# Performance work log

Hardware: AMD Instinct MI355X
Metric: run time of the kernel (lower is better)

Reference implementation:

```python
import jax, jax.numpy as jnp
import numpy as np

B, N, S = 8, 8192, 2048
IN, SKIP, OUT, EXP = 256, 128, 256, 4
GROUPS = 8


def conv1d(x, w, b):
    # 1x1 conv: x [B,C,N], w [O,C], b [O]
    return jnp.einsum('bcn,oc->bon', x, w) + b[None, :, None]


def group_norm(x, w, b, groups=GROUPS, eps=1e-5):
    Bb, C, Nn = x.shape
    xg = x.reshape(Bb, groups, C // groups, Nn)
    m = xg.mean(axis=(2, 3), keepdims=True)
    v = xg.var(axis=(2, 3), keepdims=True)
    xn = ((xg - m) * jax.lax.rsqrt(v + eps)).reshape(Bb, C, Nn)
    return xn * w[None, :, None] + b[None, :, None]


def _forward(xyz1, points1, xyz2, points2, t_emb, c_emb,
             mlp_w, mlp_b, mlp_gw, mlp_gb,
             c1w, c1b, g1w, g1b, c2w, c2b, g2w, g2b,
             tw, tb, cw, cb):
    # pairwise squared distances [B,N,S]
    dists = (-2.0 * jnp.einsum('bcn,bcm->bnm', xyz1, xyz2)
             + jnp.sum(xyz1 ** 2, axis=1)[:, :, None]
             + jnp.sum(xyz2 ** 2, axis=1)[:, None, :])
    neg_d3, idx = jax.lax.top_k(-dists, 3)          # 3 smallest distances
    d3 = -neg_d3                                     # [B,N,3]
    recip = 1.0 / (d3 + 1e-8)
    weight = recip / jnp.sum(recip, axis=2, keepdims=True)
    # gather neighbor features: points2 [B,C,S], idx [B,N,3] -> [B,C,N,3]
    gathered = jax.vmap(lambda p, i: p[:, i])(points2, idx)
    interp = jnp.sum(gathered * weight[:, None, :, :], axis=3)  # [B,IN,N]

    new_points = jnp.concatenate([points1, interp], axis=1)     # [B,IN+SKIP,N]
    x = jax.nn.silu(group_norm(conv1d(new_points, mlp_w, mlp_b), mlp_gw, mlp_gb))

    identity = x
    h = jax.nn.silu(group_norm(conv1d(x, c1w, c1b), g1w, g1b))
    h = group_norm(conv1d(h, c2w, c2b), g2w, g2b)
    st = t_emb @ tw.T + tb
    sc = c_emb @ cw.T + cb
    scale_t, shift_t = jnp.split(st, 2, axis=1)
    scale_c, shift_c = jnp.split(sc, 2, axis=1)
    scale = (scale_t + scale_c)[:, :, None]
    shift = (shift_t + shift_c)[:, :, None]
    h = h * (1.0 + scale) + shift
    return h + identity


def setup_inputs() -> dict:
    key = jax.random.key(0)
    ks = jax.random.split(key, 12)
    def rn(k, shape, s=1.0):
        return jax.random.normal(k, shape, dtype=jnp.float32) * s
    E = OUT * EXP
    return dict(
        xyz1=rn(ks[0], (B, 3, N)),
        points1=rn(ks[1], (B, SKIP, N)),
        xyz2=rn(ks[2], (B, 3, S)),
        points2=rn(ks[3], (B, IN, S)),
        t_emb=rn(ks[4], (B, OUT)),
        c_emb=rn(ks[5], (B, OUT)),
        mlp_w=rn(ks[6], (OUT, IN + SKIP), 0.02), mlp_b=jnp.zeros((OUT,), jnp.float32),
        mlp_gw=jnp.ones((OUT,), jnp.float32), mlp_gb=jnp.zeros((OUT,), jnp.float32),
        c1w=rn(ks[7], (E, OUT), 0.02), c1b=jnp.zeros((E,), jnp.float32),
        g1w=jnp.ones((E,), jnp.float32), g1b=jnp.zeros((E,), jnp.float32),
        c2w=rn(ks[8], (OUT, E), 0.02), c2b=jnp.zeros((OUT,), jnp.float32),
        g2w=jnp.ones((OUT,), jnp.float32), g2b=jnp.zeros((OUT,), jnp.float32),
        tw=rn(ks[9], (2 * OUT, OUT), 0.02), tb=jnp.zeros((2 * OUT,), jnp.float32),
        cw=rn(ks[10], (2 * OUT, OUT), 0.02), cb=jnp.zeros((2 * OUT,), jnp.float32),
    )


def reference(xyz1, points1, xyz2, points2, t_emb, c_emb,
              mlp_w, mlp_b, mlp_gw, mlp_gb,
              c1w, c1b, g1w, g1b, c2w, c2b, g2w, g2b,
              tw, tb, cw, cb):
    return _forward(xyz1, points1, xyz2, points2, t_emb, c_emb,
                    mlp_w, mlp_b, mlp_gw, mlp_gb,
                    c1w, c1b, g1w, g1b, c2w, c2b, g2w, g2b,
                    tw, tb, cw, cb)
```

## Files before the change

### kernel.cpp

```cpp
#include <hip/hip_runtime.h>
#include <hip/hip_bf16.h>

typedef unsigned short u16;
typedef __attribute__((ext_vector_type(4))) float f32x4;
typedef __attribute__((ext_vector_type(8))) short bf16x8;

typedef const __attribute__((address_space(1))) void GV;
typedef __attribute__((address_space(3))) void LV;
#define GLOAD16(g, l) __builtin_amdgcn_global_load_lds((GV*)(g), (LV*)(l), 16, 0, 0)

__device__ __forceinline__ float b2f(u16 u) {
    union { float f; unsigned int i; } v; v.i = ((unsigned int)u) << 16; return v.f;
}
__device__ __forceinline__ u16 f2b(float f) {
    union { float f; unsigned int i; } v; v.f = f;
    unsigned int x = v.i;
    return (u16)((x + 0x7fffu + ((x >> 16) & 1u)) >> 16);
}
__device__ __forceinline__ unsigned int cvt_pk_bf16(float lo, float hi) {
    unsigned int d;
    asm("v_cvt_pk_bf16_f32 %0, %1, %2" : "=v"(d) : "v"(lo), "v"(hi));
    return d;
}
__device__ __forceinline__ float silu(float t) {
    return t * __builtin_amdgcn_rcpf(1.f + __expf(-t));
}

__global__ void knn_part_kernel(const float* __restrict__ xyz1, const float* __restrict__ xyz2,
                                float2* __restrict__ cand) {
    __shared__ float4 spt[256];
    int b = blockIdx.z, ck = blockIdx.y, tid = threadIdx.x;
    const float* p2 = xyz2 + (size_t)b * 3 * 2048;
    int s0 = ck << 8;
    {
        int s = s0 + tid;
        float x = p2[s], y = p2[2048 + s], z = p2[4096 + s];
        spt[tid] = make_float4(x, y, z, (x * x + y * y) + z * z);
    }
    __syncthreads();
    int n = blockIdx.x * 256 + tid;
    const float* p1 = xyz1 + (size_t)b * 3 * 8192;
    float qx = p1[n], qy = p1[8192 + n], qz = p1[16384 + n];
    float qn = (qx * qx + qy * qy) + qz * qz;
    float d0 = 3.4e38f, d1 = 3.4e38f, d2 = 3.4e38f;
    int i0 = 0, i1 = 0, i2 = 0;
#pragma unroll 4
    for (int s = 0; s < 256; ++s) {
        float4 p = spt[s];
        float dot = (qx * p.x + qy * p.y) + qz * p.z;
        float d = (-2.f * dot + qn) + p.w;
        if (d < d2) {
            int gi = s0 + s;
            if (d < d1) {
                if (d < d0) { d2 = d1; i2 = i1; d1 = d0; i1 = i0; d0 = d; i0 = gi; }
                else        { d2 = d1; i2 = i1; d1 = d;  i1 = gi; }
            } else          { d2 = d;  i2 = gi; }
        }
    }
    float2* c = cand + (((size_t)b * 8192 + n) * 8 + ck) * 3;
    c[0] = make_float2(d0, __int_as_float(i0));
    c[1] = make_float2(d1, __int_as_float(i1));
    c[2] = make_float2(d2, __int_as_float(i2));
}

__global__ void knn_merge_kernel(const float2* __restrict__ cand,
                                 int* __restrict__ idx_out, float* __restrict__ w_out) {
    int t = blockIdx.x * 256 + threadIdx.x;
    const float2* c = cand + (size_t)t * 24;
    float d0 = 3.4e38f, d1 = 3.4e38f, d2 = 3.4e38f;
    int i0 = 0, i1 = 0, i2 = 0;
#pragma unroll
    for (int k = 0; k < 24; ++k) {
        float2 p = c[k];
        float d = p.x;
        if (d < d2) {
            int gi = __float_as_int(p.y);
            if (d < d1) {
                if (d < d0) { d2 = d1; i2 = i1; d1 = d0; i1 = i0; d0 = d; i0 = gi; }
                else        { d2 = d1; i2 = i1; d1 = d;  i1 = gi; }
            } else          { d2 = d;  i2 = gi; }
        }
    }
    float r0 = 1.f / (d0 + 1e-8f), r1 = 1.f / (d1 + 1e-8f), r2 = 1.f / (d2 + 1e-8f);
    float inv = 1.f / (r0 + r1 + r2);
    size_t base = (size_t)t * 3;
    idx_out[base] = i0; idx_out[base + 1] = i1; idx_out[base + 2] = i2;
    w_out[base] = r0 * inv; w_out[base + 1] = r1 * inv; w_out[base + 2] = r2 * inv;
}

__global__ void tr_kernel(const float* __restrict__ src, u16* __restrict__ dst,
                          int C, int S, int dstStride) {
    __shared__ u16 tile[64][70];
    int b = blockIdx.z;
    int s0 = blockIdx.x * 64, c0 = blockIdx.y * 64;
    int tid = threadIdx.x, lane = tid & 63, wv = tid >> 6;
    const float* sp = src + ((size_t)b * C + c0) * S + s0;
    for (int c = wv; c < 64; c += 4)
        tile[lane][c] = f2b(sp[(size_t)c * S + lane]);
    __syncthreads();
    u16* dp = dst + ((size_t)b * S + s0) * dstStride + c0;
    int s = tid >> 5, cp = tid & 31;
#pragma unroll
    for (int k = 0; k < 8; ++k) {
        int r = s + k * 8;
        unsigned int v = *(const unsigned int*)&tile[r][cp * 2];
        *(unsigned int*)&dp[(size_t)r * dstStride + cp * 2] = v;
    }
}

__global__ void build_x0_kernel(const u16* __restrict__ p2t,
                                const int* __restrict__ idx, const float* __restrict__ wgt,
                                u16* __restrict__ x0t) {
    int b = blockIdx.y;
    int n = blockIdx.x * 64 + (threadIdx.x >> 2);
    int q = threadIdx.x & 3;
    size_t ib = ((size_t)b * 8192 + n) * 3;
    int j0 = idx[ib], j1 = idx[ib + 1], j2 = idx[ib + 2];
    float w0 = wgt[ib], w1 = wgt[ib + 1], w2 = wgt[ib + 2];
    const u16* r0 = p2t + ((size_t)b * 2048 + j0) * 256;
    const u16* r1 = p2t + ((size_t)b * 2048 + j1) * 256;
    const u16* r2 = p2t + ((size_t)b * 2048 + j2) * 256;
    u16* out = x0t + ((size_t)b * 8192 + n) * 384;
#pragma unroll
    for (int i = 0; i < 8; ++i) {
        int c = (i * 4 + q) * 8;
        bf16x8 a0 = *(const bf16x8*)&r0[c];
        bf16x8 a1 = *(const bf16x8*)&r1[c];
        bf16x8 a2 = *(const bf16x8*)&r2[c];
        u16 ovu[8] __attribute__((aligned(16)));
#pragma unroll
        for (int j = 0; j < 8; ++j) {
            float v = w0 * b2f((u16)a0[j]) + w1 * b2f((u16)a1[j]) + w2 * b2f((u16)a2[j]);
            ovu[j] = f2b(v);
        }
        *(uint4*)&out[128 + c] = *(const uint4*)ovu;
    }
}

__global__ void cvt3_kernel(const float* __restrict__ s0, u16* __restrict__ d0, int n0,
                            const float* __restrict__ s1, u16* __restrict__ d1, int n1,
                            const float* __restrict__ s2, u16* __restrict__ d2, int n2) {
    int i = blockIdx.x * 256 + threadIdx.x;
    if (i < n0) d0[i] = f2b(s0[i]);
    if (i < n1) d1[i] = f2b(s1[i]);
    if (i < n2) d2[i] = f2b(s2[i]);
}

__global__ void film_kernel(const float* __restrict__ t_emb, const float* __restrict__ c_emb,
                            const float* __restrict__ tw, const float* __restrict__ tb,
                            const float* __restrict__ cw, const float* __restrict__ cb,
                            float* __restrict__ film) {
    __shared__ float te[256], ce[256];
    int b = blockIdx.x, tid = threadIdx.x;
    te[tid] = t_emb[b * 256 + tid];
    ce[tid] = c_emb[b * 256 + tid];
    __syncthreads();
    int j = tid + blockIdx.y * 256;
    const float* twr = tw + (size_t)j * 256;
    const float* cwr = cw + (size_t)j * 256;
    float s = 0.f;
    for (int k = 0; k < 256; ++k) s += te[k] * twr[k] + ce[k] * cwr[k];
    s += tb[j] + cb[j];
    film[b * 512 + j] = s;
}

__global__ __launch_bounds__(512, 4) void gemm_kernel(
        const u16* __restrict__ At, const u16* __restrict__ W, const float* __restrict__ bias,
        u16* __restrict__ Out, float* __restrict__ part,
        int K, int M, int gshift) {
    __shared__ u16 lA[3][128 * 32];
    __shared__ u16 lB[3][256 * 32];
    __shared__ float bpart[8][2];
    int b = blockIdx.z;
    int n0 = blockIdx.x * 128, oBase = blockIdx.y << 8;
    int tid = threadIdx.x, lane = tid & 63, wv = tid >> 6;
    int wn = wv & 1, wo = wv >> 1;
    if (tid < 16) ((float*)bpart)[tid] = 0.f;
    f32x4 acc[4][4];
#pragma unroll
    for (int i = 0; i < 4; i++)
#pragma unroll
        for (int j = 0; j < 4; j++) acc[i][j] = (f32x4){0.f, 0.f, 0.f, 0.f};

    int row = tid >> 2;
    int csrc = ((tid & 3) ^ ((row >> 1) & 3)) * 8;
    const u16* aP = At + ((size_t)b * 8192 + n0 + row) * K + csrc;
    const u16* bP0 = W + ((size_t)(oBase + row)) * K + csrc;
    const u16* bP1 = W + ((size_t)(oBase + 128 + row)) * K + csrc;
    int nK = K >> 5;
    GLOAD16(aP, &lA[0][wv * 512]);
    GLOAD16(bP0, &lB[0][wv * 512]);
    GLOAD16(bP1, &lB[0][4096 + wv * 512]);
    aP += 32; bP0 += 32; bP1 += 32;
    if (nK > 1) {
        GLOAD16(aP, &lA[1][wv * 512]);
        GLOAD16(bP0, &lB[1][wv * 512]);
        GLOAD16(bP1, &lB[1][4096 + wv * 512]);
        aP += 32; bP0 += 32; bP1 += 32;
    }
    asm volatile("s_waitcnt lgkmcnt(0)" ::: "memory");
    int cur = 0, nx1 = 1, nx2 = 2;
    int cs = lane >> 4;
    for (int kt = 0; kt < nK; ++kt) {
        if (kt + 2 < nK) {
            GLOAD16(aP, &lA[nx2][wv * 512]);
            GLOAD16(bP0, &lB[nx2][wv * 512]);
            GLOAD16(bP1, &lB[nx2][4096 + wv * 512]);
            aP += 32; bP0 += 32; bP1 += 32;
            asm volatile("s_waitcnt vmcnt(6)" ::: "memory");
        } else if (kt + 1 < nK) {
            asm volatile("s_waitcnt vmcnt(3)" ::: "memory");
        } else {
            asm volatile("s_waitcnt vmcnt(0)" ::: "memory");
        }
        __builtin_amdgcn_s_barrier();
        const u16* la = lA[cur];
        const u16* lb = lB[cur];
        bf16x8 af[4], bfr[4];
#pragma unroll
        for (int mf = 0; mf < 4; mf++) {
            int R = wn * 64 + mf * 16 + (lane & 15);
            af[mf] = *(const bf16x8*)&la[R * 32 + ((cs ^ ((R >> 1) & 3)) * 8)];
        }
#pragma unroll
        for (int nf = 0; nf < 4; nf++) {
            int R = wo * 64 + nf * 16 + (lane & 15);
            bfr[nf] = *(const bf16x8*)&lb[R * 32 + ((cs ^ ((R >> 1) & 3)) * 8)];
        }
#pragma unroll
        for (int mf = 0; mf < 4; mf++)
#pragma unroll
            for (int nf = 0; nf < 4; nf++)
                acc[mf][nf] = __builtin_amdgcn_mfma_f32_16x16x32_bf16(bfr[nf], af[mf], acc[mf][nf], 0, 0, 0);
        __builtin_amdgcn_s_barrier();
        int t = cur; cur = nx1; nx1 = nx2; nx2 = t;
    }
    int oq = (lane >> 4) * 4;
    float4 bs[4];
    float s1[4] = {0.f, 0.f, 0.f, 0.f}, s2[4] = {0.f, 0.f, 0.f, 0.f};
#pragma unroll
    for (int nf = 0; nf < 4; nf++) bs[nf] = *(const float4*)&bias[oBase + wo * 64 + nf * 16 + oq];
#pragma unroll
    for (int mf = 0; mf < 4; mf++) {
        int n = n0 + wn * 64 + mf * 16 + (lane & 15);
        u16* rowp = Out + ((size_t)b * 8192 + n) * M + oBase + wo * 64 + oq;
#pragma unroll
        for (int nf = 0; nf < 4; nf++) {
            float v0 = acc[mf][nf][0] + bs[nf].x;
            float v1 = acc[mf][nf][1] + bs[nf].y;
            float v2 = acc[mf][nf][2] + bs[nf].z;
            float v3 = acc[mf][nf][3] + bs[nf].w;
            s1[nf] += (v0 + v1) + (v2 + v3);
            s2[nf] += (v0 * v0 + v1 * v1) + (v2 * v2 + v3 * v3);
            uint2 pk;
            pk.x = cvt_pk_bf16(v0, v1);
            pk.y = cvt_pk_bf16(v2, v3);
            *(uint2*)&rowp[nf * 16] = pk;
        }
    }
#pragma unroll
    for (int nf = 0; nf < 4; nf++) {
        float a = s1[nf], c = s2[nf];
#pragma unroll
        for (int off = 32; off > 0; off >>= 1) {
            a += __shfl_xor(a, off, 64);
            c += __shfl_xor(c, off, 64);
        }
        if (lane == 0) {
            int gl = (wo * 64 + nf * 16) >> gshift;
            atomicAdd(&bpart[gl][0], a);
            atomicAdd(&bpart[gl][1], c);
        }
    }
    __syncthreads();
    int nlg = 256 >> gshift;
    if (tid < 2 * nlg) {
        int gl = tid >> 1, s = tid & 1;
        int g = (oBase >> gshift) + gl;
        part[(((size_t)b * 8 + g) * 2 + s) * 64 + blockIdx.x] = bpart[gl][s];
    }
}

__global__ __launch_bounds__(512, 4) void gemm_gn_kernel(
        const u16* __restrict__ At, const u16* __restrict__ W, const float* __restrict__ bias,
        const float* __restrict__ tab,
        u16* __restrict__ Out, float* __restrict__ part,
        int K, int M, int gshift) {
    __shared__ u16 lA[2][128 * 32];
    __shared__ u16 lB[2][256 * 32];
    __shared__ float cA[1024], cB[1024];
    __shared__ float bpart[8][2];
    int b = blockIdx.z;
    int n0 = blockIdx.x * 128, oBase = blockIdx.y << 8;
    int tid = threadIdx.x, lane = tid & 63, wv = tid >> 6;
    int wn = wv & 1, wo = wv >> 1;
    if (tid < 16) ((float*)bpart)[tid] = 0.f;
    f32x4 acc[4][4];
#pragma unroll
    for (int i = 0; i < 4; i++)
#pragma unroll
        for (int j = 0; j < 4; j++) acc[i][j] = (f32x4){0.f, 0.f, 0.f, 0.f};

    int row = tid >> 2;
    int csrc = ((tid & 3) ^ ((row >> 1) & 3)) * 8;
    const u16* aP = At + ((size_t)b * 8192 + n0 + row) * K + csrc;
    const u16* bP0 = W + ((size_t)(oBase + row)) * K + csrc;
    const u16* bP1 = W + ((size_t)(oBase + 128 + row)) * K + csrc;
    int nK = K >> 5;
    uint4 areg = *(const uint4*)aP; aP += 32;
    GLOAD16(bP0, &lB[0][wv * 512]);
    GLOAD16(bP1, &lB[0][4096 + wv * 512]);
    bP0 += 32; bP1 += 32;
    {
        const float* tA = tab + (size_t)b * K;
        const float* tB = tab + (size_t)(8 + b) * K;
        for (int i = tid; i < K; i += 512) { cA[i] = tA[i]; cB[i] = tB[i]; }
    }
    __syncthreads();
    {
        int c = csrc;
        const u16* rr = (const u16*)&areg;
        float4 a0 = *(const float4*)&cA[c], a1 = *(const float4*)&cA[c + 4];
        float4 b0 = *(const float4*)&cB[c], b1 = *(const float4*)&cB[c + 4];
        float va[8] = {a0.x, a0.y, a0.z, a0.w, a1.x, a1.y, a1.z, a1.w};
        float vb[8] = {b0.x, b0.y, b0.z, b0.w, b1.x, b1.y, b1.z, b1.w};
        float v[8];
#pragma unroll
        for (int j = 0; j < 8; ++j) v[j] = silu(b2f(rr[j]) * va[j] + vb[j]);
        uint4 o;
        o.x = cvt_pk_bf16(v[0], v[1]); o.y = cvt_pk_bf16(v[2], v[3]);
        o.z = cvt_pk_bf16(v[4], v[5]); o.w = cvt_pk_bf16(v[6], v[7]);
        *(uint4*)&lA[0][tid * 8] = o;
    }
    asm volatile("s_waitcnt vmcnt(0) lgkmcnt(0)" ::: "memory");
    __builtin_amdgcn_s_barrier();
    int cur = 0;
    int cs = lane >> 4;
    for (int kt = 0; kt < nK; ++kt) {
        if (kt + 1 < nK) {
            areg = *(const uint4*)aP; aP += 32;
            GLOAD16(bP0, &lB[cur ^ 1][wv * 512]);
            GLOAD16(bP1, &lB[cur ^ 1][4096 + wv * 512]);
            bP0 += 32; bP1 += 32;
        }
        const u16* la = lA[cur];
        const u16* lb = lB[cur];
        bf16x8 af[4], bfr[4];
#pragma unroll
        for (int mf = 0; mf < 4; mf++) {
            int R = wn * 64 + mf * 16 + (lane & 15);
            af[mf] = *(const bf16x8*)&la[R * 32 + ((cs ^ ((R >> 1) & 3)) * 8)];
        }
#pragma unroll
        for (int nf = 0; nf < 4; nf++) {
            int R = wo * 64 + nf * 16 + (lane & 15);
            bfr[nf] = *(const bf16x8*)&lb[R * 32 + ((cs ^ ((R >> 1) & 3)) * 8)];
        }
#pragma unroll
        for (int mf = 0; mf < 4; mf++)
#pragma unroll
            for (int nf = 0; nf < 4; nf++)
                acc[mf][nf] = __builtin_amdgcn_mfma_f32_16x16x32_bf16(bfr[nf], af[mf], acc[mf][nf], 0, 0, 0);
        if (kt + 1 < nK) {
            int c = (kt + 1) * 32 + csrc;
            const u16* rr = (const u16*)&areg;
            float4 a0 = *(const float4*)&cA[c], a1 = *(const float4*)&cA[c + 4];
            float4 b0 = *(const float4*)&cB[c], b1 = *(const float4*)&cB[c + 4];
            float va[8] = {a0.x, a0.y, a0.z, a0.w, a1.x, a1.y, a1.z, a1.w};
            float vb[8] = {b0.x, b0.y, b0.z, b0.w, b1.x, b1.y, b1.z, b1.w};
            float v[8];
#pragma unroll
            for (int j = 0; j < 8; ++j) v[j] = silu(b2f(rr[j]) * va[j] + vb[j]);
            uint4 o;
            o.x = cvt_pk_bf16(v[0], v[1]); o.y = cvt_pk_bf16(v[2], v[3]);
            o.z = cvt_pk_bf16(v[4], v[5]); o.w = cvt_pk_bf16(v[6], v[7]);
            *(uint4*)&lA[cur ^ 1][tid * 8] = o;
            asm volatile("s_waitcnt vmcnt(0)" ::: "memory");
        }
        asm volatile("s_waitcnt lgkmcnt(0)" ::: "memory");
        __builtin_amdgcn_s_barrier();
        cur ^= 1;
    }
    int oq = (lane >> 4) * 4;
    float4 bs[4];
    float s1[4] = {0.f, 0.f, 0.f, 0.f}, s2[4] = {0.f, 0.f, 0.f, 0.f};
#pragma unroll
    for (int nf = 0; nf < 4; nf++) bs[nf] = *(const float4*)&bias[oBase + wo * 64 + nf * 16 + oq];
#pragma unroll
    for (int mf = 0; mf < 4; mf++) {
        int n = n0 + wn * 64 + mf * 16 + (lane & 15);
        u16* rowp = Out + ((size_t)b * 8192 + n) * M + oBase + wo * 64 + oq;
#pragma unroll
        for (int nf = 0; nf < 4; nf++) {
            float v0 = acc[mf][nf][0] + bs[nf].x;
            float v1 = acc[mf][nf][1] + bs[nf].y;
            float v2 = acc[mf][nf][2] + bs[nf].z;
            float v3 = acc[mf][nf][3] + bs[nf].w;
            s1[nf] += (v0 + v1) + (v2 + v3);
            s2[nf] += (v0 * v0 + v1 * v1) + (v2 * v2 + v3 * v3);
            uint2 pk;
            pk.x = cvt_pk_bf16(v0, v1);
            pk.y = cvt_pk_bf16(v2, v3);
            *(uint2*)&rowp[nf * 16] = pk;
        }
    }
#pragma unroll
    for (int nf = 0; nf < 4; nf++) {
        float a = s1[nf], c = s2[nf];
#pragma unroll
        for (int off = 32; off > 0; off >>= 1) {
            a += __shfl_xor(a, off, 64);
            c += __shfl_xor(c, off, 64);
        }
        if (lane == 0) {
            int gl = (wo * 64 + nf * 16) >> gshift;
            atomicAdd(&bpart[gl][0], a);
            atomicAdd(&bpart[gl][1], c);
        }
    }
    __syncthreads();
    int nlg = 256 >> gshift;
    if (tid < 2 * nlg) {
        int gl = tid >> 1, s = tid & 1;
        int g = (oBase >> gshift) + gl;
        part[(((size_t)b * 8 + g) * 2 + s) * 64 + blockIdx.x] = bpart[gl][s];
    }
}

__global__ void gn_stats_coef_kernel(const float* __restrict__ part,
                                     const float* __restrict__ gw, const float* __restrict__ gb,
                                     float* __restrict__ stats, float* __restrict__ tab,
                                     int K, int gshift, float invCnt) {
    __shared__ float sg[16];
    int b = blockIdx.y, c0 = blockIdx.x * 256, tid = threadIdx.x;
    int ng = 256 >> gshift;
    if (tid < 2 * ng) {
        int gl = tid >> 1, s = tid & 1;
        int g = (c0 >> gshift) + gl;
        const float* p = part + (((size_t)b * 8 + g) * 2 + s) * 64;
        float sum = 0.f;
#pragma unroll
        for (int i = 0; i < 64; i += 4) {
            float4 v = *(const float4*)&p[i];
            sum += (v.x + v.y) + (v.z + v.w);
        }
        sg[gl * 2 + s] = sum;
        stats[((size_t)b * 8 + g) * 2 + s] = sum;
    }
    __syncthreads();
    int c = c0 + tid;
    int gl = tid >> gshift;
    float sum = sg[gl * 2], ssq = sg[gl * 2 + 1];
    float m = sum * invCnt;
    float rstd = rsqrtf(fmaxf(ssq * invCnt - m * m, 0.f) + 1e-5f);
    float A = rstd * gw[c];
    tab[(size_t)b * K + c] = A;
    tab[(size_t)(8 + b) * K + c] = gb[c] - m * A;
}

__global__ void gn_reduce_kernel(const float* __restrict__ part, float* __restrict__ stats) {
    int t = threadIdx.x;
    const float4* p = (const float4*)(part + (size_t)t * 64);
    float s = 0.f;
#pragma unroll
    for (int i = 0; i < 16; i++) { float4 v = p[i]; s += (v.x + v.y) + (v.z + v.w); }
    stats[t] = s;
}

__global__ void gn_apply_kernel(const u16* __restrict__ Yin, u16* __restrict__ Yout,
                                const float* __restrict__ tab) {
    int t = blockIdx.x * 256 + threadIdx.x;
    int c8 = t & 31, c0 = c8 << 3;
    int row0 = t >> 5;
    int rowstep = (gridDim.x * 256) >> 5;
    float A[8], Bc[8];
    int bprev = -1;
    for (int row = row0; row < 65536; row += rowstep) {
        int b = row >> 13;
        if (b != bprev) {
            bprev = b;
            float4 a0 = *(const float4*)(tab + (size_t)b * 256 + c0);
            float4 a1 = *(const float4*)(tab + (size_t)b * 256 + c0 + 4);
            float4 b0 = *(const float4*)(tab + (size_t)(8 + b) * 256 + c0);
            float4 b1 = *(const float4*)(tab + (size_t)(8 + b) * 256 + c0 + 4);
            A[0]=a0.x;A[1]=a0.y;A[2]=a0.z;A[3]=a0.w;A[4]=a1.x;A[5]=a1.y;A[6]=a1.z;A[7]=a1.w;
            Bc[0]=b0.x;Bc[1]=b0.y;Bc[2]=b0.z;Bc[3]=b0.w;Bc[4]=b1.x;Bc[5]=b1.y;Bc[6]=b1.z;Bc[7]=b1.w;
        }
        size_t off = ((size_t)row << 8) + c0;
        uint4 v4 = *(const uint4*)(Yin + off);
        const u16* vu = (const u16*)&v4;
        float v[8];
#pragma unroll
        for (int j = 0; j < 8; j++) v[j] = silu(b2f(vu[j]) * A[j] + Bc[j]);
        uint4 o;
        o.x = cvt_pk_bf16(v[0], v[1]); o.y = cvt_pk_bf16(v[2], v[3]);
        o.z = cvt_pk_bf16(v[4], v[5]); o.w = cvt_pk_bf16(v[6], v[7]);
        *(uint4*)(Yout + off) = o;
    }
}

__global__ void final_kernel(const u16* __restrict__ Y2, const u16* __restrict__ Xraw,
                             const float* __restrict__ g0w, const float* __restrict__ g0b,
                             const float* __restrict__ stats0,
                             const float* __restrict__ g2w, const float* __restrict__ g2b,
                             const float* __restrict__ stats2, const float* __restrict__ film,
                             float* __restrict__ out) {
    __shared__ float tile[64][257];
    int b = blockIdx.y, n0 = blockIdx.x * 64, tid = threadIdx.x;
    const float invCnt = 1.f / (32.f * 8192.f);
    int c8 = tid & 31, c0 = c8 << 3, g = c8 >> 2;
    float sum = stats2[(b * 8 + g) * 2], ssq = stats2[(b * 8 + g) * 2 + 1];
    float m = sum * invCnt, rstd = rsqrtf(fmaxf(ssq * invCnt - m * m, 0.f) + 1e-5f);
    float sum0 = stats0[(b * 8 + g) * 2], ssq0 = stats0[(b * 8 + g) * 2 + 1];
    float m0 = sum0 * invCnt, rstd0 = rsqrtf(fmaxf(ssq0 * invCnt - m0 * m0, 0.f) + 1e-5f);
    float4 w0 = *(const float4*)(g2w + c0), w1 = *(const float4*)(g2w + c0 + 4);
    float4 q0 = *(const float4*)(g2b + c0), q1 = *(const float4*)(g2b + c0 + 4);
    float4 f0 = *(const float4*)(film + b * 512 + c0), f1 = *(const float4*)(film + b * 512 + c0 + 4);
    float4 h0 = *(const float4*)(film + b * 512 + 256 + c0), h1 = *(const float4*)(film + b * 512 + 256 + c0 + 4);
    float4 u0 = *(const float4*)(g0w + c0), u1 = *(const float4*)(g0w + c0 + 4);
    float4 e0 = *(const float4*)(g0b + c0), e1 = *(const float4*)(g0b + c0 + 4);
    float wv[8] = {w0.x, w0.y, w0.z, w0.w, w1.x, w1.y, w1.z, w1.w};
    float qv[8] = {q0.x, q0.y, q0.z, q0.w, q1.x, q1.y, q1.z, q1.w};
    float fs[8] = {f0.x, f0.y, f0.z, f0.w, f1.x, f1.y, f1.z, f1.w};
    float fh[8] = {h0.x, h0.y, h0.z, h0.w, h1.x, h1.y, h1.z, h1.w};
    float uv[8] = {u0.x, u0.y, u0.z, u0.w, u1.x, u1.y, u1.z, u1.w};
    float ev[8] = {e0.x, e0.y, e0.z, e0.w, e1.x, e1.y, e1.z, e1.w};
    float A[8], Bc[8], A0[8], B0[8];
#pragma unroll
    for (int j = 0; j < 8; j++) {
        float sc = 1.f + fs[j];
        A[j] = rstd * wv[j] * sc;
        Bc[j] = (qv[j] - m * rstd * wv[j]) * sc + fh[j];
        A0[j] = rstd0 * uv[j];
        B0[j] = ev[j] - m0 * A0[j];
    }
    int nrb = tid >> 5;
#pragma unroll
    for (int k = 0; k < 8; k++) {
        int nr = nrb + k * 8;
        size_t base = ((size_t)b * 8192 + n0 + nr) * 256 + c0;
        uint4 yv = *(const uint4*)(Y2 + base);
        uint4 xv = *(const uint4*)(Xraw + base);
        const u16* yy = (const u16*)&yv;
        const u16* xx = (const u16*)&xv;
#pragma unroll
        for (int j = 0; j < 8; j++) {
            float x = silu(b2f(xx[j]) * A0[j] + B0[j]);
            tile[nr][c0 + j] = b2f(yy[j]) * A[j] + Bc[j] + x;
        }
    }
    __syncthreads();
    for (int q = tid; q < 256 * 16; q += 256) {
        int c = q >> 4, n4 = q & 15;
        float4 o;
        o.x = tile[n4 * 4 + 0][c];
        o.y = tile[n4 * 4 + 1][c];
        o.z = tile[n4 * 4 + 2][c];
        o.w = tile[n4 * 4 + 3][c];
        *(float4*)&out[((size_t)b * 256 + c) * 8192 + n0 + n4 * 4] = o;
    }
}

extern "C" void kernel_launch(void* const* d_in, const int* in_sizes, int n_in,
                              void* d_out, int out_size, void* d_ws, size_t ws_size,
                              hipStream_t stream) {
    const float* xyz1    = (const float*)d_in[0];
    const float* points1 = (const float*)d_in[1];
    const float* xyz2    = (const float*)d_in[2];
    const float* points2 = (const float*)d_in[3];
    const float* t_emb   = (const float*)d_in[4];
    const float* c_emb   = (const float*)d_in[5];
    const float* mlp_w   = (const float*)d_in[6];
    const float* mlp_b   = (const float*)d_in[7];
    const float* mlp_gw  = (const float*)d_in[8];
    const float* mlp_gb  = (const float*)d_in[9];
    const float* c1w     = (const float*)d_in[10];
    const float* c1b     = (const float*)d_in[11];
    const float* g1w     = (const float*)d_in[12];
    const float* g1b     = (const float*)d_in[13];
    const float* c2w     = (const float*)d_in[14];
    const float* c2b     = (const float*)d_in[15];
    const float* g2w     = (const float*)d_in[16];
    const float* g2b     = (const float*)d_in[17];
    const float* tw      = (const float*)d_in[18];
    const float* tb      = (const float*)d_in[19];
    const float* cw      = (const float*)d_in[20];
    const float* cb      = (const float*)d_in[21];

    char* ws = (char*)d_ws;
    int*   idx    = (int*)ws;
    float* wgt    = (float*)(ws + 786432);
    float* stats0 = (float*)(ws + 1572864);
    float* stats1 = (float*)(ws + 1573376);
    float* stats2 = (float*)(ws + 1573888);
    float* film   = (float*)(ws + 1574400);
    float* part0  = (float*)(ws + 1590784);
    float* part1  = (float*)(ws + 1623552);
    float* part2  = (float*)(ws + 1656320);
    u16* wb_mlp   = (u16*)(ws + 1689088);
    u16* wb_c1    = (u16*)(ws + 1885696);
    u16* wb_c2    = (u16*)(ws + 2409984);
    float* tab0   = (float*)(ws + 2934272);
    float* tab1   = (float*)(ws + 2950656);
    u16* X0t = (u16*)(ws + 4194304);
    u16* Y1t = (u16*)(ws + 54525952);
    u16* H1t = (u16*)(ws + 88080384);
    u16* Y2t = X0t;
    u16* Y1act = X0t;
    float2* cand = (float2*)X0t;
    u16* p2t = H1t;
    float* out = (float*)d_out;

    cvt3_kernel<<<1024, 256, 0, stream>>>(mlp_w, wb_mlp, 98304,
                                          c1w, wb_c1, 262144, c2w, wb_c2, 262144);
    knn_part_kernel<<<dim3(32, 8, 8), 256, 0, stream>>>(xyz1, xyz2, cand);
    knn_merge_kernel<<<256, 256, 0, stream>>>(cand, idx, wgt);
    tr_kernel<<<dim3(128, 2, 8), 256, 0, stream>>>(points1, X0t, 128, 8192, 384);
    tr_kernel<<<dim3(32, 4, 8), 256, 0, stream>>>(points2, p2t, 256, 2048, 256);
    build_x0_kernel<<<dim3(128, 8), 256, 0, stream>>>(p2t, idx, wgt, X0t);
    film_kernel<<<dim3(8, 2), 256, 0, stream>>>(t_emb, c_emb, tw, tb, cw, cb, film);
    gemm_kernel<<<dim3(64, 1, 8), 512, 0, stream>>>(X0t, wb_mlp, mlp_b, Y1t, part0, 384, 256, 5);
    gn_stats_coef_kernel<<<dim3(1, 8), 256, 0, stream>>>(part0, mlp_gw, mlp_gb, stats0, tab0,
                                                         256, 5, 1.f / (32.f * 8192.f));
    gn_apply_kernel<<<512, 256, 0, stream>>>(Y1t, Y1act, tab0);
    gemm_kernel<<<dim3(64, 4, 8), 512, 0, stream>>>(Y1act, wb_c1, c1b, H1t, part1, 256, 1024, 7);
    gn_stats_coef_kernel<<<dim3(4, 8), 256, 0, stream>>>(part1, g1w, g1b, stats1, tab1,
                                                         1024, 7, 1.f / (128.f * 8192.f));
    gemm_gn_kernel<<<dim3(64, 1, 8), 512, 0, stream>>>(H1t, wb_c2, c2b, tab1, Y2t, part2, 1024, 256, 5);
    gn_reduce_kernel<<<1, 128, 0, stream>>>(part2, stats2);
    final_kernel<<<dim3(128, 8), 256, 0, stream>>>(Y2t, Y1t, mlp_gw, mlp_gb, stats0,
                                                   g2w, g2b, stats2, film, out);
}
```

Measured before the change: 334.6 us.

## Fuse kNN merge into gather, add nontemporal GEMM loads/stores, widen final stores

```diff
diff --git a/kernel.cpp b/kernel.cpp
--- a/kernel.cpp
+++ b/kernel.cpp
@@ -4,6 +4,8 @@
 typedef unsigned short u16;
 typedef __attribute__((ext_vector_type(4))) float f32x4;
 typedef __attribute__((ext_vector_type(8))) short bf16x8;
+typedef __attribute__((ext_vector_type(2))) unsigned int u32x2;
+typedef __attribute__((ext_vector_type(4))) unsigned int u32x4;
 
 typedef const __attribute__((address_space(1))) void GV;
 typedef __attribute__((address_space(3))) void LV;
@@ -63,10 +65,32 @@
     c[2] = make_float2(d2, __int_as_float(i2));
 }
 
-__global__ void knn_merge_kernel(const float2* __restrict__ cand,
-                                 int* __restrict__ idx_out, float* __restrict__ w_out) {
-    int t = blockIdx.x * 256 + threadIdx.x;
-    const float2* c = cand + (size_t)t * 24;
+__global__ void tr_kernel(const float* __restrict__ src, u16* __restrict__ dst,
+                          int C, int S, int dstStride) {
+    __shared__ u16 tile[64][70];
+    int b = blockIdx.z;
+    int s0 = blockIdx.x * 64, c0 = blockIdx.y * 64;
+    int tid = threadIdx.x, lane = tid & 63, wv = tid >> 6;
+    const float* sp = src + ((size_t)b * C + c0) * S + s0;
+    for (int c = wv; c < 64; c += 4)
+        tile[lane][c] = f2b(sp[(size_t)c * S + lane]);
+    __syncthreads();
+    u16* dp = dst + ((size_t)b * S + s0) * dstStride + c0;
+    int s = tid >> 5, cp = tid & 31;
+#pragma unroll
+    for (int k = 0; k < 8; ++k) {
+        int r = s + k * 8;
+        unsigned int v = *(const unsigned int*)&tile[r][cp * 2];
+        *(unsigned int*)&dp[(size_t)r * dstStride + cp * 2] = v;
+    }
+}
+
+__global__ void build_x0_kernel(const u16* __restrict__ p2t, const float2* __restrict__ cand,
+                                u16* __restrict__ x0t) {
+    int b = blockIdx.y;
+    int n = blockIdx.x * 64 + (threadIdx.x >> 2);
+    int q = threadIdx.x & 3;
+    const float2* c = cand + ((size_t)b * 8192 + n) * 24;
     float d0 = 3.4e38f, d1 = 3.4e38f, d2 = 3.4e38f;
     int i0 = 0, i1 = 0, i2 = 0;
 #pragma unroll
@@ -81,59 +105,26 @@
             } else          { d2 = d;  i2 = gi; }
         }
     }
-    float r0 = 1.f / (d0 + 1e-8f), r1 = 1.f / (d1 + 1e-8f), r2 = 1.f / (d2 + 1e-8f);
-    float inv = 1.f / (r0 + r1 + r2);
-    size_t base = (size_t)t * 3;
-    idx_out[base] = i0; idx_out[base + 1] = i1; idx_out[base + 2] = i2;
-    w_out[base] = r0 * inv; w_out[base + 1] = r1 * inv; w_out[base + 2] = r2 * inv;
-}
-
-__global__ void tr_kernel(const float* __restrict__ src, u16* __restrict__ dst,
-                          int C, int S, int dstStride) {
-    __shared__ u16 tile[64][70];
-    int b = blockIdx.z;
-    int s0 = blockIdx.x * 64, c0 = blockIdx.y * 64;
-    int tid = threadIdx.x, lane = tid & 63, wv = tid >> 6;
-    const float* sp = src + ((size_t)b * C + c0) * S + s0;
-    for (int c = wv; c < 64; c += 4)
-        tile[lane][c] = f2b(sp[(size_t)c * S + lane]);
-    __syncthreads();
-    u16* dp = dst + ((size_t)b * S + s0) * dstStride + c0;
-    int s = tid >> 5, cp = tid & 31;
-#pragma unroll
-    for (int k = 0; k < 8; ++k) {
-        int r = s + k * 8;
-        unsigned int v = *(const unsigned int*)&tile[r][cp * 2];
-        *(unsigned int*)&dp[(size_t)r * dstStride + cp * 2] = v;
-    }
-}
-
-__global__ void build_x0_kernel(const u16* __restrict__ p2t,
-                                const int* __restrict__ idx, const float* __restrict__ wgt,
-                                u16* __restrict__ x0t) {
-    int b = blockIdx.y;
-    int n = blockIdx.x * 64 + (threadIdx.x >> 2);
-    int q = threadIdx.x & 3;
-    size_t ib = ((size_t)b * 8192 + n) * 3;
-    int j0 = idx[ib], j1 = idx[ib + 1], j2 = idx[ib + 2];
-    float w0 = wgt[ib], w1 = wgt[ib + 1], w2 = wgt[ib + 2];
-    const u16* r0 = p2t + ((size_t)b * 2048 + j0) * 256;
-    const u16* r1 = p2t + ((size_t)b * 2048 + j1) * 256;
-    const u16* r2 = p2t + ((size_t)b * 2048 + j2) * 256;
+    float r0w = 1.f / (d0 + 1e-8f), r1w = 1.f / (d1 + 1e-8f), r2w = 1.f / (d2 + 1e-8f);
+    float inv = 1.f / (r0w + r1w + r2w);
+    float w0 = r0w * inv, w1 = r1w * inv, w2 = r2w * inv;
+    const u16* r0 = p2t + ((size_t)b * 2048 + i0) * 256;
+    const u16* r1 = p2t + ((size_t)b * 2048 + i1) * 256;
+    const u16* r2 = p2t + ((size_t)b * 2048 + i2) * 256;
     u16* out = x0t + ((size_t)b * 8192 + n) * 384;
 #pragma unroll
     for (int i = 0; i < 8; ++i) {
-        int c = (i * 4 + q) * 8;
-        bf16x8 a0 = *(const bf16x8*)&r0[c];
-        bf16x8 a1 = *(const bf16x8*)&r1[c];
-        bf16x8 a2 = *(const bf16x8*)&r2[c];
+        int cc = (i * 4 + q) * 8;
+        bf16x8 a0 = *(const bf16x8*)&r0[cc];
+        bf16x8 a1 = *(const bf16x8*)&r1[cc];
+        bf16x8 a2 = *(const bf16x8*)&r2[cc];
         u16 ovu[8] __attribute__((aligned(16)));
 #pragma unroll
         for (int j = 0; j < 8; ++j) {
             float v = w0 * b2f((u16)a0[j]) + w1 * b2f((u16)a1[j]) + w2 * b2f((u16)a2[j]);
             ovu[j] = f2b(v);
         }
-        *(uint4*)&out[128 + c] = *(const uint4*)ovu;
+        *(uint4*)&out[128 + cc] = *(const uint4*)ovu;
     }
 }
 
@@ -164,6 +155,7 @@
     film[b * 512 + j] = s;
 }
 
+template<int NTS>
 __global__ __launch_bounds__(512, 4) void gemm_kernel(
         const u16* __restrict__ At, const u16* __restrict__ W, const float* __restrict__ bias,
         u16* __restrict__ Out, float* __restrict__ part,
@@ -252,10 +244,11 @@
             float v3 = acc[mf][nf][3] + bs[nf].w;
             s1[nf] += (v0 + v1) + (v2 + v3);
             s2[nf] += (v0 * v0 + v1 * v1) + (v2 * v2 + v3 * v3);
-            uint2 pk;
+            u32x2 pk;
             pk.x = cvt_pk_bf16(v0, v1);
             pk.y = cvt_pk_bf16(v2, v3);
-            *(uint2*)&rowp[nf * 16] = pk;
+            if (NTS) __builtin_nontemporal_store(pk, (u32x2*)&rowp[nf * 16]);
+            else *(u32x2*)&rowp[nf * 16] = pk;
         }
     }
 #pragma unroll
@@ -307,7 +300,7 @@
     const u16* bP0 = W + ((size_t)(oBase + row)) * K + csrc;
     const u16* bP1 = W + ((size_t)(oBase + 128 + row)) * K + csrc;
     int nK = K >> 5;
-    uint4 areg = *(const uint4*)aP; aP += 32;
+    u32x4 areg = __builtin_nontemporal_load((const u32x4*)aP); aP += 32;
     GLOAD16(bP0, &lB[0][wv * 512]);
     GLOAD16(bP1, &lB[0][4096 + wv * 512]);
     bP0 += 32; bP1 += 32;
@@ -338,7 +331,7 @@
     int cs = lane >> 4;
     for (int kt = 0; kt < nK; ++kt) {
         if (kt + 1 < nK) {
-            areg = *(const uint4*)aP; aP += 32;
+            areg = __builtin_nontemporal_load((const u32x4*)aP); aP += 32;
             GLOAD16(bP0, &lB[cur ^ 1][wv * 512]);
             GLOAD16(bP1, &lB[cur ^ 1][4096 + wv * 512]);
             bP0 += 32; bP1 += 32;
@@ -550,14 +543,19 @@
         }
     }
     __syncthreads();
-    for (int q = tid; q < 256 * 16; q += 256) {
-        int c = q >> 4, n4 = q & 15;
-        float4 o;
-        o.x = tile[n4 * 4 + 0][c];
-        o.y = tile[n4 * 4 + 1][c];
-        o.z = tile[n4 * 4 + 2][c];
-        o.w = tile[n4 * 4 + 3][c];
-        *(float4*)&out[((size_t)b * 256 + c) * 8192 + n0 + n4 * 4] = o;
+    for (int q = tid; q < 256 * 4; q += 256) {
+        int c = q >> 2, n16 = q & 3;
+        float4* dst = (float4*)&out[((size_t)b * 256 + c) * 8192 + n0 + n16 * 16];
+#pragma unroll
+        for (int j = 0; j < 4; j++) {
+            int n = n16 * 16 + j * 4;
+            float4 o;
+            o.x = tile[n + 0][c];
+            o.y = tile[n + 1][c];
+            o.z = tile[n + 2][c];
+            o.w = tile[n + 3][c];
+            dst[j] = o;
+        }
     }
 }
 
@@ -588,8 +586,6 @@
     const float* cb      = (const float*)d_in[21];
 
     char* ws = (char*)d_ws;
-    int*   idx    = (int*)ws;
-    float* wgt    = (float*)(ws + 786432);
     float* stats0 = (float*)(ws + 1572864);
     float* stats1 = (float*)(ws + 1573376);
     float* stats2 = (float*)(ws + 1573888);
@@ -607,23 +603,22 @@
     u16* H1t = (u16*)(ws + 88080384);
     u16* Y2t = X0t;
     u16* Y1act = X0t;
-    float2* cand = (float2*)X0t;
     u16* p2t = H1t;
+    float2* cand = (float2*)(H1t + 8388608ull);
     float* out = (float*)d_out;
 
     cvt3_kernel<<<1024, 256, 0, stream>>>(mlp_w, wb_mlp, 98304,
                                           c1w, wb_c1, 262144, c2w, wb_c2, 262144);
     knn_part_kernel<<<dim3(32, 8, 8), 256, 0, stream>>>(xyz1, xyz2, cand);
-    knn_merge_kernel<<<256, 256, 0, stream>>>(cand, idx, wgt);
     tr_kernel<<<dim3(128, 2, 8), 256, 0, stream>>>(points1, X0t, 128, 8192, 384);
     tr_kernel<<<dim3(32, 4, 8), 256, 0, stream>>>(points2, p2t, 256, 2048, 256);
-    build_x0_kernel<<<dim3(128, 8), 256, 0, stream>>>(p2t, idx, wgt, X0t);
+    build_x0_kernel<<<dim3(128, 8), 256, 0, stream>>>(p2t, cand, X0t);
     film_kernel<<<dim3(8, 2), 256, 0, stream>>>(t_emb, c_emb, tw, tb, cw, cb, film);
-    gemm_kernel<<<dim3(64, 1, 8), 512, 0, stream>>>(X0t, wb_mlp, mlp_b, Y1t, part0, 384, 256, 5);
+    gemm_kernel<0><<<dim3(64, 1, 8), 512, 0, stream>>>(X0t, wb_mlp, mlp_b, Y1t, part0, 384, 256, 5);
     gn_stats_coef_kernel<<<dim3(1, 8), 256, 0, stream>>>(part0, mlp_gw, mlp_gb, stats0, tab0,
                                                          256, 5, 1.f / (32.f * 8192.f));
     gn_apply_kernel<<<512, 256, 0, stream>>>(Y1t, Y1act, tab0);
-    gemm_kernel<<<dim3(64, 4, 8), 512, 0, stream>>>(Y1act, wb_c1, c1b, H1t, part1, 256, 1024, 7);
+    gemm_kernel<1><<<dim3(64, 4, 8), 512, 0, stream>>>(Y1act, wb_c1, c1b, H1t, part1, 256, 1024, 7);
     gn_stats_coef_kernel<<<dim3(4, 8), 256, 0, stream>>>(part1, g1w, g1b, stats1, tab1,
                                                          1024, 7, 1.f / (128.f * 8192.f));
     gemm_gn_kernel<<<dim3(64, 1, 8), 512, 0, stream>>>(H1t, wb_c2, c2b, tab1, Y2t, part2, 1024, 256, 5);
```

New measurement: 362.1 us. 1.08x slower.
